# Performance work log

Measured on AMD Instinct MI355X. Metric: run time of the kernel, lower is better.

Reference implementation:

```python
import jax, jax.numpy as jnp
import numpy as np

N_HEADS, INPUT_DIM, EMBED_DIM = 8, 128, 128
KEY_DIM = EMBED_DIM // N_HEADS  # val_dim = key_dim = 16
B, N = 8, 1024


def setup_inputs() -> dict:
    key = jax.random.key(0)
    ks = jax.random.split(key, 16)
    stdv_k = 1.0 / np.sqrt(KEY_DIM)
    stdv_e = 1.0 / np.sqrt(EMBED_DIM)

    def U(k, shape, s):
        return jax.random.uniform(k, shape, jnp.float32, -s, s)

    hdk = (N_HEADS, INPUT_DIM, KEY_DIM)
    hke = (N_HEADS, KEY_DIM, EMBED_DIM)
    return {
        "q_n": jax.random.normal(ks[0], (B, N, INPUT_DIM), jnp.float32),
        "q_c": jax.random.normal(ks[1], (B, N, INPUT_DIM), jnp.float32),
        "mask": jax.random.bernoulli(ks[2], 0.5, (B, N, N)),
        "W_query_n": U(ks[3], hdk, stdv_k),
        "W_key_nn": U(ks[4], hdk, stdv_k),
        "W_val_nn": U(ks[5], hdk, stdv_k),
        "W_key_c": U(ks[6], hdk, stdv_k),
        "W_val_c": U(ks[7], hdk, stdv_k),
        "W_query_c": U(ks[8], hdk, stdv_k),
        "W_key_n": U(ks[9], hdk, stdv_k),
        "W_val_n": U(ks[10], hdk, stdv_k),
        "W_out_node": U(ks[11], hke, stdv_e),
        "W_out_color": U(ks[12], hke, stdv_e),
    }


def reference(q_n, q_c, mask, W_query_n, W_key_nn, W_val_nn, W_key_c, W_val_c,
              W_query_c, W_key_n, W_val_n, W_out_node, W_out_color):
    norm = 1.0 / jnp.sqrt(jnp.asarray(KEY_DIM, q_n.dtype))
    neg_inf = jnp.asarray(-jnp.inf, q_n.dtype)

    def proj(x, W):  # (B,N,D), (H,D,K) -> (H,B,N,K)
        return jnp.einsum('bnd,hdk->hbnk', x, W)

    # --- color stream: q_c attends over nodes q_n ---
    Q_c = proj(q_c, W_query_c)
    K_n = proj(q_n, W_key_n)
    V_n = proj(q_n, W_val_n)
    attn_c = jax.nn.softmax(norm * jnp.einsum('hbqk,hbnk->hbqn', Q_c, K_n), axis=-1)
    heads_c = jnp.einsum('hbqn,hbnv->hbqv', attn_c, V_n)
    out_color = jnp.einsum('hbqv,hve->bqe', heads_c, W_out_color)

    # --- node stream: masked self-attention + attention over colors ---
    Q_n = proj(q_n, W_query_n)
    K_nn = proj(q_n, W_key_nn)
    V_nn = proj(q_n, W_val_nn)
    comp_nn = norm * jnp.einsum('hbqk,hbnk->hbqn', Q_n, K_nn)
    m = mask[None]  # (1,B,Q,N) broadcast over heads; True = not allowed
    comp_nn = jnp.where(m, neg_inf, comp_nn)
    attn_nn = jax.nn.softmax(comp_nn, axis=-1)
    attn_nn = jnp.where(m, jnp.asarray(0.0, q_n.dtype), attn_nn)
    heads_nn = jnp.einsum('hbqn,hbnv->hbqv', attn_nn, V_nn)

    K_nc = proj(q_c, W_key_c)
    V_nc = proj(q_c, W_val_c)
    attn_nc = jax.nn.softmax(norm * jnp.einsum('hbqk,hbnk->hbqn', Q_n, K_nc), axis=-1)
    heads_nc = jnp.einsum('hbqn,hbnv->hbqv', attn_nc, V_nc)

    heads = heads_nn + heads_nc
    out = jnp.einsum('hbqv,hve->bqe', heads, W_out_node)
    return (out, out_color)
```

## Files before the change

kernel.cpp:

```cpp
#include <hip/hip_runtime.h>
#include <stdint.h>

#define NH 8
#define NB 8
#define NN 1024
#define ND 128
#define NK 16
#define NF (NB*NN)
#define C2EXP 0.36067376022224085f
#define LSTR 136

typedef float f32x16 __attribute__((ext_vector_type(16)));
typedef short bf16x8 __attribute__((ext_vector_type(8)));

__device__ __forceinline__ uint16_t f2bf(float f){
  uint32_t x = __float_as_uint(f);
  uint32_t r = (x + 0x7fffu + ((x>>16)&1u)) >> 16;
  return (uint16_t)r;
}
__device__ __forceinline__ float fast_exp2(float x){
#if __has_builtin(__builtin_amdgcn_exp2f)
  return __builtin_amdgcn_exp2f(x);
#else
  return exp2f(x);
#endif
}

__global__ __launch_bounds__(256) void pack_kernel(const int* __restrict__ mask,
                                                   uint32_t* __restrict__ packN,
                                                   uint16_t* __restrict__ onesw){
  if (blockIdx.x == 0) {
    for (int i = threadIdx.x; i < 1024; i += 256) onesw[i] = 0x3F80;
  }
  const int w = threadIdx.x >> 6, lane = threadIdx.x & 63;
  const int row = blockIdx.x*4 + w;
  const int* mp = mask + (size_t)row*NN;
  uint32_t* dst = packN + (size_t)row*32;
  for (int wq = 0; wq < 16; ++wq) {
    int v = mp[wq*64 + lane];
    unsigned long long bal = __ballot(v != 0);
    if (lane == 0) { dst[wq*2] = (uint32_t)bal; dst[wq*2+1] = (uint32_t)(bal>>32); }
  }
}

struct ProjArgs { const float* x[8]; const float* w[8]; };

__global__ __launch_bounds__(512, 4) void proj_kernel(ProjArgs args, uint16_t* ws){
  __shared__ __align__(16) uint16_t WT[128*LSTR];
  __shared__ __align__(16) uint16_t S[128*LSTR];
  const int p = blockIdx.y;
  const int rb = blockIdx.x;
  const int tid = threadIdx.x;

  const float4* w4 = (const float4*)args.w[p];
  #pragma unroll
  for (int i = 0; i < 8; ++i) {
    int e4 = i*512 + tid;
    float4 f = w4[e4];
    int e = e4*4;
    int h = e >> 11, d = (e >> 4) & 127, k = e & 15;
    uint16_t* wr = &WT[(h*16 + k)*LSTR + d];
    wr[0*LSTR] = f2bf(f.x); wr[1*LSTR] = f2bf(f.y);
    wr[2*LSTR] = f2bf(f.z); wr[3*LSTR] = f2bf(f.w);
  }
  __syncthreads();

  const int wave = tid >> 6, lane = tid & 63;
  const int l5 = lane >> 5, lm = lane & 31;
  const int rt = wave & 3, nh2 = wave >> 2;
  const int r0 = rb*128 + rt*32;
  const float* xrow = args.x[p] + (size_t)(r0 + lm)*ND + l5*8;

  bf16x8 afr[8];
  #pragma unroll
  for (int kt = 0; kt < 8; ++kt) {
    float4 f0 = *(const float4*)(xrow + kt*16);
    float4 f1 = *(const float4*)(xrow + kt*16 + 4);
    bf16x8 a;
    a[0]=f2bf(f0.x); a[1]=f2bf(f0.y); a[2]=f2bf(f0.z); a[3]=f2bf(f0.w);
    a[4]=f2bf(f1.x); a[5]=f2bf(f1.y); a[6]=f2bf(f1.z); a[7]=f2bf(f1.w);
    afr[kt] = a;
  }

  const bool tr = (p==2)|(p==5)|(p==7);
  const float qsc = (p==0 || p==3) ? C2EXP : 1.0f;
  #pragma unroll
  for (int nt2 = 0; nt2 < 2; ++nt2) {
    const int nt = nh2*2 + nt2;
    f32x16 acc;
    #pragma unroll
    for (int i = 0; i < 16; ++i) acc[i] = 0.f;
    #pragma unroll
    for (int kt = 0; kt < 8; ++kt) {
      bf16x8 b = *(const bf16x8*)(&WT[(nt*32 + lm)*LSTR + kt*16 + l5*8]);
      acc = __builtin_amdgcn_mfma_f32_32x32x16_bf16(afr[kt], b, acc, 0, 0, 0);
    }
    #pragma unroll
    for (int i = 0; i < 16; ++i) {
      int r = rt*32 + (i&3) + 8*(i>>2) + 4*l5;
      int c = nt*32 + lm;
      if (tr) {
        int t2 = (r>>2)&3;
        int rp = (t2==1 || t2==2) ? (r^12) : r;
        S[c*LSTR + rp] = f2bf(acc[i]);
      } else {
        S[r*LSTR + c] = f2bf(acc[i]*qsc);
      }
    }
  }
  __syncthreads();

  uint16_t* dst = ws + (size_t)p*((size_t)NH*NF*NK);
  if (!tr) {
    #pragma unroll
    for (int it = 0; it < 4; ++it) {
      int c = it*512 + tid;
      int row = c >> 4, cg = c & 15;
      bf16x8 v = *(const bf16x8*)(&S[row*LSTR + cg*8]);
      int h = cg >> 1, k8 = cg & 1;
      *(bf16x8*)(dst + ((size_t)h*NF + rb*128 + row)*NK + k8*8) = v;
    }
  } else {
    const int b = rb >> 3, nb = (rb & 7)*128;
    #pragma unroll
    for (int it = 0; it < 4; ++it) {
      int c = it*512 + tid;
      int col = c >> 4, ng = c & 15;
      bf16x8 v = *(const bf16x8*)(&S[col*LSTR + ng*8]);
      int h = col >> 4, k = col & 15;
      *(bf16x8*)(dst + ((size_t)(h*NB + b)*NK + k)*NN + nb + ng*8) = v;
    }
  }
}

template<bool MASKED>
__device__ __forceinline__ void attn_stream(
    const uint16_t* __restrict__ kp, bf16x8 aq,
    const uint16_t* __restrict__ vbase, const uint4* __restrict__ pmw4,
    int nh, int l5, int lm, f32x16& O)
{
  f32x16 Z;
  #pragma unroll
  for (int i = 0; i < 16; ++i) Z[i] = 0.f;

  const int base_n = nh*512;
  const bool vload = (lm < 17);
  const uint16_t* kl = kp + (size_t)(base_n + lm)*NK + l5*8;
  const uint16_t* vl = vbase + base_n + l5*8;

  bf16x8 kf_c = *(const bf16x8*)(kl);
  bf16x8 kf_n;
  uint4 mq, mqn;
  if (MASKED) { mq = pmw4[nh*4]; mqn = mq; }

  bf16x8 av1, av2;
  #pragma unroll
  for (int i = 0; i < 8; ++i) { av1[i]=0; av2[i]=0; }

  #pragma unroll
  for (int t = 0; t < 16; ++t) {
    if (vload) {
      const uint16_t* vp = vl + t*32;
      av1 = *(const bf16x8*)(vp);
      av2 = *(const bf16x8*)(vp + 16);
    }
    if (t < 15) kf_n = *(const bf16x8*)(kl + (t+1)*512);
    if (MASKED && (t&3)==0 && t < 12) mqn = pmw4[nh*4 + (t>>2) + 1];

    f32x16 St = __builtin_amdgcn_mfma_f32_32x32x16_bf16(kf_c, aq, Z, 0, 0, 0);

    uint32_t mws = 0u;
    if (MASKED) {
      uint32_t w = ((t&3)==0) ? mq.x : ((t&3)==1) ? mq.y
                 : ((t&3)==2) ? mq.z : mq.w;
      mws = w >> (4*l5);
    }
    union { uint32_t u[4]; bf16x8 v; } B1, B2;
    #pragma unroll
    for (int k = 0; k < 4; ++k) {
      float p0 = fast_exp2(St[2*k]);
      float p1 = fast_exp2(St[2*k+1]);
      float p8 = fast_exp2(St[2*k+8]);
      float p9 = fast_exp2(St[2*k+9]);
      if (MASKED) {
        const int i0 = 2*k, i1 = 2*k+1, i8 = 2*k+8, i9 = 2*k+9;
        if ((mws >> ((i0&3) + 8*(i0>>2))) & 1u) p0 = 0.f;
        if ((mws >> ((i1&3) + 8*(i1>>2))) & 1u) p1 = 0.f;
        if ((mws >> ((i8&3) + 8*(i8>>2))) & 1u) p8 = 0.f;
        if ((mws >> ((i9&3) + 8*(i9>>2))) & 1u) p9 = 0.f;
      }
      B1.u[k] = __builtin_amdgcn_perm(__float_as_uint(p1),
                                      __float_as_uint(p0), 0x07060302u);
      B2.u[k] = __builtin_amdgcn_perm(__float_as_uint(p9),
                                      __float_as_uint(p8), 0x07060302u);
    }
    O = __builtin_amdgcn_mfma_f32_32x32x16_bf16(av1, B1.v, O, 0, 0, 0);
    O = __builtin_amdgcn_mfma_f32_32x32x16_bf16(av2, B2.v, O, 0, 0, 0);

    kf_c = kf_n;
    if (MASKED && (t&3)==3) mq = mqn;
  }
}

__global__ __launch_bounds__(256, 5) void attn_kernel(
    const uint16_t* __restrict__ Qn_, const uint16_t* __restrict__ Knn,
    const uint16_t* __restrict__ VTnn, const uint16_t* __restrict__ Knc,
    const uint16_t* __restrict__ VTnc,
    const uint16_t* __restrict__ Qc_, const uint16_t* __restrict__ Kn,
    const uint16_t* __restrict__ VTn,
    const uint32_t* __restrict__ packN, const uint16_t* __restrict__ onesb,
    uint16_t* __restrict__ hnn_, uint16_t* __restrict__ hnc_,
    uint16_t* __restrict__ hc_)
{
  __shared__ float cw[1152];
  const int z = blockIdx.z;
  const uint16_t* Q  = (z == 2) ? Qc_ : Qn_;
  const uint16_t* K  = (z == 0) ? Knn : (z == 1) ? Knc : Kn;
  const uint16_t* VT = (z == 0) ? VTnn : (z == 1) ? VTnc : VTn;
  uint16_t* outp     = (z == 0) ? hnn_ : (z == 1) ? hnc_ : hc_;

  const int h = blockIdx.x >> 3, b = blockIdx.x & 7;
  const int hb = h*8 + b;
  const size_t base = ((size_t)h*NF + (size_t)b*NN)*NK;
  const int tid = threadIdx.x;

  const int wave = tid >> 6, lane = tid & 63;
  const int l5 = lane >> 5, lm = lane & 31;
  const int qt = wave & 1, nh = wave >> 1;
  const int q = blockIdx.y*64 + qt*32 + lm;

  const bf16x8 aq = *(const bf16x8*)(Q + base + (size_t)q*NK + l5*8);
  const uint4* pmw4 = (const uint4*)(packN + ((size_t)b*NN + q)*32);

  const uint16_t* VTb = VT + (size_t)hb*(NK*NN);
  const uint16_t* vb = (lm < 16) ? (VTb + (size_t)lm*NN) : onesb;

  f32x16 O;
  #pragma unroll
  for (int i = 0; i < 16; ++i) O[i] = 0.f;

  if (z == 0) attn_stream<true >(K + base, aq, vb, pmw4,   nh, l5, lm, O);
  else        attn_stream<false>(K + base, aq, vb, nullptr, nh, l5, lm, O);

  float L1 = O[8] + __shfl_xor(O[8], 32, 64);

  float* cwp = cw + (size_t)((qt*2 + l5)*32 + lm)*9;
  if (nh == 1) {
    #pragma unroll
    for (int i = 0; i < 8; ++i) cwp[i] = O[i];
    cwp[8] = L1;
  }
  __syncthreads();
  if (nh == 0) {
    const float l1 = L1 + cwp[8];
    const float i1 = (l1 > 0.f) ? 1.f/l1 : 0.f;
    uint32_t w[4];
    #pragma unroll
    for (int k = 0; k < 4; ++k) {
      float va = (O[2*k]   + cwp[2*k])  *i1;
      float vb2 = (O[2*k+1] + cwp[2*k+1])*i1;
      w[k] = ((uint32_t)f2bf(vb2) << 16) | f2bf(va);
    }
    uint16_t* hp = outp + ((size_t)b*NN + q)*128 + h*16 + l5*4;
    *(uint2*)(hp)     = make_uint2(w[0], w[1]);
    *(uint2*)(hp + 8) = make_uint2(w[2], w[3]);
  }
}

__global__ __launch_bounds__(512, 4) void outproj_kernel(
    const uint16_t* __restrict__ hnn, const uint16_t* __restrict__ hnc,
    const uint16_t* __restrict__ hc,
    const float* __restrict__ wn, const float* __restrict__ wc,
    float* __restrict__ out)
{
  __shared__ __align__(16) uint16_t WT[128*LSTR];
  const int s = blockIdx.y;
  const int rb = blockIdx.x;
  const int tid = threadIdx.x;
  const float* wsrc = s ? wc : wn;
  const float4* w4 = (const float4*)wsrc;
  #pragma unroll
  for (int i = 0; i < 8; ++i) {
    int e4 = i*512 + tid;
    float4 f = w4[e4];
    int e = e4*4;
    int c = e >> 7, col = e & 127;
    uint16_t* wr = &WT[col*LSTR + c];
    wr[0*LSTR] = f2bf(f.x); wr[1*LSTR] = f2bf(f.y);
    wr[2*LSTR] = f2bf(f.z); wr[3*LSTR] = f2bf(f.w);
  }
  __syncthreads();

  const int wave = tid >> 6, lane = tid & 63;
  const int l5 = lane >> 5, lm = lane & 31;
  const int rt = wave >> 2, nt = wave & 3;
  const int r0 = rb*64 + rt*32;
  const size_t hoff = (size_t)(r0 + lm)*128 + l5*8;
  const uint16_t* hp1 = (s ? hc : hnn) + hoff;
  bf16x8 afr[8], afr2[8];
  #pragma unroll
  for (int kt = 0; kt < 8; ++kt) afr[kt] = *(const bf16x8*)(hp1 + kt*16);
  if (!s) {
    const uint16_t* hp2 = hnc + hoff;
    #pragma unroll
    for (int kt = 0; kt < 8; ++kt) afr2[kt] = *(const bf16x8*)(hp2 + kt*16);
  }

  float* dst = out + (size_t)s*((size_t)NF*ND) + (size_t)r0*ND;
  f32x16 acc;
  #pragma unroll
  for (int i = 0; i < 16; ++i) acc[i] = 0.f;
  #pragma unroll
  for (int kt = 0; kt < 8; ++kt) {
    bf16x8 b = *(const bf16x8*)(&WT[(nt*32 + lm)*LSTR + kt*16 + l5*8]);
    acc = __builtin_amdgcn_mfma_f32_32x32x16_bf16(afr[kt], b, acc, 0, 0, 0);
    if (!s) acc = __builtin_amdgcn_mfma_f32_32x32x16_bf16(afr2[kt], b, acc, 0, 0, 0);
  }
  #pragma unroll
  for (int i = 0; i < 16; ++i) {
    int r = (i&3) + 8*(i>>2) + 4*l5;
    dst[(size_t)r*ND + nt*32 + lm] = acc[i];
  }
}

extern "C" void kernel_launch(void* const* d_in, const int* in_sizes, int n_in,
                              void* d_out, int out_size, void* d_ws, size_t ws_size,
                              hipStream_t stream)
{
  const float* q_n = (const float*)d_in[0];
  const float* q_c = (const float*)d_in[1];
  const int* mask = (const int*)d_in[2];
  const float* W[10];
  for (int i = 0; i < 10; ++i) W[i] = (const float*)d_in[3+i];

  uint16_t* ws16 = (uint16_t*)d_ws;
  const size_t PE = (size_t)NH*NF*NK;
  uint16_t* Qc   = ws16 + 0*PE;
  uint16_t* Kn   = ws16 + 1*PE;
  uint16_t* VTn  = ws16 + 2*PE;
  uint16_t* Qn   = ws16 + 3*PE;
  uint16_t* Knn  = ws16 + 4*PE;
  uint16_t* VTnn = ws16 + 5*PE;
  uint16_t* Knc  = ws16 + 6*PE;
  uint16_t* VTnc = ws16 + 7*PE;
  uint16_t* hnn  = ws16 + 8*PE;
  uint32_t* packN   = (uint32_t*)(ws16 + 9*PE);
  uint16_t* onesb   = ws16 + 9*PE + 524288;
  uint16_t* hc   = ws16 + 10*PE;
  uint16_t* hnc  = ws16 + 11*PE;

  pack_kernel<<<2048, 256, 0, stream>>>(mask, packN, onesb);

  ProjArgs pa;
  pa.x[0]=q_c; pa.w[0]=W[5];
  pa.x[1]=q_n; pa.w[1]=W[6];
  pa.x[2]=q_n; pa.w[2]=W[7];
  pa.x[3]=q_n; pa.w[3]=W[0];
  pa.x[4]=q_n; pa.w[4]=W[1];
  pa.x[5]=q_n; pa.w[5]=W[2];
  pa.x[6]=q_c; pa.w[6]=W[3];
  pa.x[7]=q_c; pa.w[7]=W[4];
  proj_kernel<<<dim3(64, 8), 512, 0, stream>>>(pa, ws16);

  attn_kernel<<<dim3(64, 16, 3), 256, 0, stream>>>(
      Qn, Knn, VTnn, Knc, VTnc, Qc, Kn, VTn, packN, onesb,
      hnn, hnc, hc);

  outproj_kernel<<<dim3(128, 2), 512, 0, stream>>>(hnn, hnc, hc,
                                                   W[8], W[9], (float*)d_out);
}
```

Measured before the change: 168.8 us.

## Tile transposed V into 32-key blocks and prefetch V fragments one step ahead

New measurement: 164.7 us. 1.02x faster.

```diff
diff --git a/kernel.cpp b/kernel.cpp
--- a/kernel.cpp
+++ b/kernel.cpp
@@ -30,7 +30,7 @@
                                                    uint32_t* __restrict__ packN,
                                                    uint16_t* __restrict__ onesw){
   if (blockIdx.x == 0) {
-    for (int i = threadIdx.x; i < 1024; i += 256) onesw[i] = 0x3F80;
+    for (int i = threadIdx.x; i < 16384; i += 256) onesw[i] = 0x3F80;
   }
   const int w = threadIdx.x >> 6, lane = threadIdx.x & 63;
   const int row = blockIdx.x*4 + w;
@@ -128,7 +128,9 @@
       int col = c >> 4, ng = c & 15;
       bf16x8 v = *(const bf16x8*)(&S[col*LSTR + ng*8]);
       int h = col >> 4, k = col & 15;
-      *(bf16x8*)(dst + ((size_t)(h*NB + b)*NK + k)*NN + nb + ng*8) = v;
+      int pn = nb + ng*8;
+      *(bf16x8*)(dst + (size_t)(h*NB + b)*16384
+                     + (size_t)(pn >> 5)*512 + k*32 + (pn & 31)) = v;
     }
   }
 }
@@ -136,7 +138,7 @@
 template<bool MASKED>
 __device__ __forceinline__ void attn_stream(
     const uint16_t* __restrict__ kp, bf16x8 aq,
-    const uint16_t* __restrict__ vbase, const uint4* __restrict__ pmw4,
+    const uint16_t* __restrict__ vb, const uint4* __restrict__ pmw4,
     int nh, int l5, int lm, f32x16& O)
 {
   f32x16 Z;
@@ -146,25 +148,32 @@
   const int base_n = nh*512;
   const bool vload = (lm < 17);
   const uint16_t* kl = kp + (size_t)(base_n + lm)*NK + l5*8;
-  const uint16_t* vl = vbase + base_n + l5*8;
+  const uint16_t* vl = vb + (size_t)nh*8192 + l5*8;
+
+  uint4 mq, mqn;
+  if (MASKED) { mq = pmw4[nh*4]; mqn = mq; }
+
+  bf16x8 av1, av2, av1n, av2n;
+  #pragma unroll
+  for (int i = 0; i < 8; ++i) { av1[i]=0; av2[i]=0; av1n[i]=0; av2n[i]=0; }
 
   bf16x8 kf_c = *(const bf16x8*)(kl);
   bf16x8 kf_n;
-  uint4 mq, mqn;
-  if (MASKED) { mq = pmw4[nh*4]; mqn = mq; }
-
-  bf16x8 av1, av2;
-  #pragma unroll
-  for (int i = 0; i < 8; ++i) { av1[i]=0; av2[i]=0; }
+  if (vload) {
+    av1 = *(const bf16x8*)(vl);
+    av2 = *(const bf16x8*)(vl + 16);
+  }
 
   #pragma unroll
   for (int t = 0; t < 16; ++t) {
-    if (vload) {
-      const uint16_t* vp = vl + t*32;
-      av1 = *(const bf16x8*)(vp);
-      av2 = *(const bf16x8*)(vp + 16);
-    }
-    if (t < 15) kf_n = *(const bf16x8*)(kl + (t+1)*512);
+    if (t < 15) {
+      if (vload) {
+        const uint16_t* vp = vl + (t+1)*512;
+        av1n = *(const bf16x8*)(vp);
+        av2n = *(const bf16x8*)(vp + 16);
+      }
+      kf_n = *(const bf16x8*)(kl + (t+1)*512);
+    }
     if (MASKED && (t&3)==0 && t < 12) mqn = pmw4[nh*4 + (t>>2) + 1];
 
     f32x16 St = __builtin_amdgcn_mfma_f32_32x32x16_bf16(kf_c, aq, Z, 0, 0, 0);
@@ -197,7 +206,7 @@
     O = __builtin_amdgcn_mfma_f32_32x32x16_bf16(av1, B1.v, O, 0, 0, 0);
     O = __builtin_amdgcn_mfma_f32_32x32x16_bf16(av2, B2.v, O, 0, 0, 0);
 
-    kf_c = kf_n;
+    if (t < 15) { kf_c = kf_n; av1 = av1n; av2 = av2n; }
     if (MASKED && (t&3)==3) mq = mqn;
   }
 }
@@ -233,7 +242,7 @@
   const uint4* pmw4 = (const uint4*)(packN + ((size_t)b*NN + q)*32);
 
   const uint16_t* VTb = VT + (size_t)hb*(NK*NN);
-  const uint16_t* vb = (lm < 16) ? (VTb + (size_t)lm*NN) : onesb;
+  const uint16_t* vb = (lm < 16) ? (VTb + (size_t)lm*32) : onesb;
 
   f32x16 O;
   #pragma unroll
```
